# Optimization experiments

Hardware: AMD Instinct MI355X
Metric: run time of the kernel (lower is better)

Reference implementation:

```python
import jax, jax.numpy as jnp
import numpy as np

B, S, D = 8, 4096, 256
L, H = 4, 8
HD = D // H  # head_dim = 32
EPS = 1e-5


def layer_norm(x, gamma, beta):
    mu = jnp.mean(x, axis=-1, keepdims=True)
    var = jnp.mean(jnp.square(x - mu), axis=-1, keepdims=True)
    return (x - mu) * jax.lax.rsqrt(var + EPS) * gamma + beta


def setup_inputs() -> dict:
    key = jax.random.key(0)
    ks = jax.random.split(key, 9)
    sc = 0.02
    x = jax.random.normal(ks[0], (B, S, D), dtype=jnp.float32)
    # per-head projection weights, torch Linear convention: (out=head_dim, in=D)
    Wq = jax.random.normal(ks[1], (L, H, HD, D), dtype=jnp.float32) * sc
    Wk = jax.random.normal(ks[2], (L, H, HD, D), dtype=jnp.float32) * sc
    Wv = jax.random.normal(ks[3], (L, H, HD, D), dtype=jnp.float32) * sc
    W1 = jax.random.normal(ks[4], (L, D, D), dtype=jnp.float32) * sc
    b1 = jax.random.normal(ks[5], (L, D), dtype=jnp.float32) * sc
    W2 = jax.random.normal(ks[6], (L, D, D), dtype=jnp.float32) * sc
    b2 = jax.random.normal(ks[7], (L, D), dtype=jnp.float32) * sc
    gamma = jnp.ones((D,), dtype=jnp.float32)
    beta = jnp.zeros((D,), dtype=jnp.float32)
    return {"processed_grid_repr": x, "Wq": Wq, "Wk": Wk, "Wv": Wv,
            "W1": W1, "b1": b1, "W2": W2, "b2": b2,
            "gamma": gamma, "beta": beta}


def reference(processed_grid_repr, Wq, Wk, Wv, W1, b1, W2, b2, gamma, beta):
    out = processed_grid_repr  # (B, S, D)
    scale = 1.0 / jnp.sqrt(jnp.float32(S))  # original scales by sqrt(seq_len)
    for l in range(L):
        h = layer_norm(out, gamma, beta)
        # all heads at once: (B, H, S, HD)
        Q = jnp.einsum('bsd,hed->bhse', h, Wq[l])
        K = jnp.einsum('bsd,hed->bhse', h, Wk[l])
        V = jnp.einsum('bsd,hed->bhse', h, Wv[l])
        # original does key.reshape(B, HD, S) (a RESHAPE, not a transpose)
        Kr = K.reshape(B, H, HD, S)
        # original einsum 'bqq,bqd->bqd' only uses the diagonal of QK^r,
        # so compute only the diagonal: diag[b,h,q] = sum_e Q[b,h,q,e]*Kr[b,h,e,q]
        diag = jnp.einsum('bhse,bhes->bhs', Q, Kr) * scale
        attn = diag[..., None] * V  # (B, H, S, HD)
        # concat heads along last dim (head order preserved)
        msa_out = attn.transpose(0, 2, 1, 3).reshape(B, S, D)
        attended = msa_out + out
        m = layer_norm(attended, gamma, beta)
        m = jax.nn.gelu(m @ W1[l].T + b1[l], approximate=False)
        m = jax.nn.gelu(m @ W2[l].T + b2[l], approximate=False)
        out = m + attended
    # final: layer norm of CLS-like token 0
    return layer_norm(out[:, 0, :], gamma, beta)  # (B, D)
```

## Files before the change

kernel.cpp:

```cpp
#include <hip/hip_runtime.h>
#include <hip/hip_bf16.h>
#include <hip/hip_fp16.h>

typedef _Float16 half_t;
typedef _Float16 half8 __attribute__((ext_vector_type(8)));
typedef _Float16 half4 __attribute__((ext_vector_type(4)));
typedef float f32x4 __attribute__((ext_vector_type(4)));

#define BB 8
#define SS 4096
#define DD 256
#define HH 8
#define LL 4
#define MTOT (BB*SS)

__device__ inline float gelu_f(float v) { return 0.5f * v * (1.0f + erff(v * 0.70710678118f)); }

__device__ __forceinline__ void gload16(const half_t* g, half_t* l) {
    __builtin_amdgcn_global_load_lds(
        (const __attribute__((address_space(1))) void*)g,
        (__attribute__((address_space(3))) void*)l, 16, 0, 0);
}

__global__ __launch_bounds__(256) void prep_weights(
    const float* __restrict__ Wq, const float* __restrict__ Wk, const float* __restrict__ Wv,
    const float* __restrict__ W1, const float* __restrict__ b1,
    const float* __restrict__ W2, const float* __restrict__ b2,
    const float* __restrict__ gamma, const float* __restrict__ beta,
    half_t* __restrict__ Wall, half_t* __restrict__ W1h, half_t* __restrict__ W2h,
    float* __restrict__ bqkv, float* __restrict__ b1f, float* __restrict__ b2f)
{
    int blk = blockIdx.x;
    int l = blk / 5, type = blk % 5;
    int o = threadIdx.x;
    const float* src = (type == 0 ? Wq : type == 1 ? Wk : type == 2 ? Wv : type == 3 ? W1 : W2)
                       + ((size_t)l * 256 + o) * 256;
    half_t* dsth = (type < 3) ? Wall + ((size_t)(l * 3 + type) * 256 + o) * 256
                 : (type == 3) ? W1h + ((size_t)l * 256 + o) * 256
                               : W2h + ((size_t)l * 256 + o) * 256;
    float acc = 0.f;
    for (int d4 = 0; d4 < 64; ++d4) {
        float4 w = *(const float4*)(src + d4 * 4);
        half4 hv;
        if (type == 4) {
            hv = half4{ (half_t)w.x, (half_t)w.y, (half_t)w.z, (half_t)w.w };
        } else {
            float4 g = *(const float4*)(gamma + d4 * 4);
            float4 bt = *(const float4*)(beta + d4 * 4);
            acc += w.x * bt.x + w.y * bt.y + w.z * bt.z + w.w * bt.w;
            hv = half4{ (half_t)(w.x * g.x), (half_t)(w.y * g.y), (half_t)(w.z * g.z), (half_t)(w.w * g.w) };
        }
        *(half4*)(dsth + d4 * 4) = hv;
    }
    if (type < 3) bqkv[(l * 3 + type) * 256 + o] = acc;
    else if (type == 3) b1f[l * 256 + o] = b1[l * 256 + o] + acc;
    else b2f[l * 256 + o] = b2[l * 256 + o];
}

__global__ __launch_bounds__(256) void cvt_x(const float* __restrict__ in, half_t* __restrict__ out) {
    int i = (blockIdx.x * 256 + threadIdx.x) * 4;
    float4 v = *(const float4*)(in + i);
    half4 h = { (half_t)v.x, (half_t)v.y, (half_t)v.z, (half_t)v.w };
    *(half4*)(out + i) = h;
}

__global__ __launch_bounds__(256) void ln_z(const half_t* __restrict__ in, half_t* __restrict__ z) {
    int wave = threadIdx.x >> 6, lane = threadIdx.x & 63;
    int row = blockIdx.x * 4 + wave;
    size_t base = (size_t)row * DD + lane * 4;
    half4 x4 = *(const half4*)(in + base);
    float a0 = x4[0], a1 = x4[1], a2 = x4[2], a3 = x4[3];
    float s1 = a0 + a1 + a2 + a3;
    float s2 = a0 * a0 + a1 * a1 + a2 * a2 + a3 * a3;
    #pragma unroll
    for (int m = 32; m; m >>= 1) {
        s1 += __shfl_xor(s1, m);
        s2 += __shfl_xor(s2, m);
    }
    float mu = s1 * (1.0f / DD);
    float var = s2 * (1.0f / DD) - mu * mu;
    float rs = rsqrtf(var + 1e-5f);
    half4 o = { (half_t)((a0 - mu) * rs), (half_t)((a1 - mu) * rs),
                (half_t)((a2 - mu) * rs), (half_t)((a3 - mu) * rs) };
    *(half4*)(z + base) = o;
}

__device__ inline void xcd_remap(int& bx, int& by, int& bz) {
    int lin = blockIdx.x + gridDim.x * (blockIdx.y + gridDim.y * blockIdx.z);
    int nyz = gridDim.y * gridDim.z;
    int xcd = lin & 7;
    int slot = lin >> 3;
    int yz = slot % nyz;
    int xi = slot / nyz;
    bx = xcd + 8 * xi;
    by = yz % gridDim.y;
    bz = yz / gridDim.y;
}

template<int EPI>
__global__ __launch_bounds__(256) void gemm64(const half_t* __restrict__ A,
                                              const half_t* __restrict__ Wbase,
                                              const float* __restrict__ biasBase,
                                              const half_t* __restrict__ resid,
                                              half_t* __restrict__ o0,
                                              half_t* __restrict__ o1,
                                              half_t* __restrict__ o2) {
    const int t = threadIdx.x, lane = t & 63, wavei = t >> 6;
    const int wm = wavei >> 1, wn = wavei & 1, r = lane & 15, g = lane >> 4;
    int bx, by, bz;
    xcd_remap(bx, by, bz);
    const int row0 = bx * 64, col0 = by * 64;
    const half_t* W = Wbase + (size_t)bz * 65536;
    const float* bias = biasBase + bz * 256;
    half_t* outp = (bz == 0) ? o0 : ((bz == 1) ? o1 : o2);

    __shared__ __align__(16) half_t ldsA[2][4096];
    __shared__ __align__(16) half_t ldsB[2][4096];

    const half_t* Ag = A + (size_t)row0 * DD;
    const half_t* Wg = W + (size_t)col0 * DD;

    int rowS[2], chS[2];
    #pragma unroll
    for (int i = 0; i < 2; ++i) {
        int G = i * 256 + t;
        rowS[i] = G >> 3;
        chS[i] = ((G & 7) ^ (rowS[i] & 7)) * 8;
    }

    #pragma unroll
    for (int i = 0; i < 2; ++i) {
        int G = i * 256 + t;
        gload16(Ag + (size_t)rowS[i] * DD + chS[i], &ldsA[0][G * 8]);
        gload16(Wg + (size_t)rowS[i] * DD + chS[i], &ldsB[0][G * 8]);
    }
    __syncthreads();

    f32x4 acc[2][2];
    #pragma unroll
    for (int i = 0; i < 2; ++i)
        #pragma unroll
        for (int j = 0; j < 2; ++j) acc[i][j] = (f32x4){0.f, 0.f, 0.f, 0.f};

    #pragma unroll
    for (int stp = 0; stp < 4; ++stp) {
        const int cur = stp & 1;
        if (stp < 3) {
            int kk = (stp + 1) * 64;
            #pragma unroll
            for (int i = 0; i < 2; ++i) {
                int G = i * 256 + t;
                gload16(Ag + (size_t)rowS[i] * DD + kk + chS[i], &ldsA[cur ^ 1][G * 8]);
                gload16(Wg + (size_t)rowS[i] * DD + kk + chS[i], &ldsB[cur ^ 1][G * 8]);
            }
        }
        #pragma unroll
        for (int ks = 0; ks < 2; ++ks) {
            half8 af[2], bf[2];
            #pragma unroll
            for (int mt = 0; mt < 2; ++mt) {
                int rw = wm * 32 + mt * 16 + r;
                int cc = (ks * 4 + g) ^ (rw & 7);
                af[mt] = *(const half8*)&ldsA[cur][rw * 64 + cc * 8];
            }
            #pragma unroll
            for (int nt = 0; nt < 2; ++nt) {
                int rw = wn * 32 + nt * 16 + r;
                int cc = (ks * 4 + g) ^ (rw & 7);
                bf[nt] = *(const half8*)&ldsB[cur][rw * 64 + cc * 8];
            }
            #pragma unroll
            for (int mt = 0; mt < 2; ++mt)
                #pragma unroll
                for (int nt = 0; nt < 2; ++nt)
                    acc[mt][nt] = __builtin_amdgcn_mfma_f32_16x16x32_f16(af[mt], bf[nt], acc[mt][nt], 0, 0, 0);
        }
        __syncthreads();
    }

    half_t* ldsT = &ldsA[0][0];
    #pragma unroll
    for (int mt = 0; mt < 2; ++mt) {
        #pragma unroll
        for (int nt = 0; nt < 2; ++nt) {
            int colL = wn * 32 + nt * 16 + r;
            float bv = bias[col0 + colL];
            #pragma unroll
            for (int j = 0; j < 4; ++j) {
                int rowL = wm * 32 + mt * 16 + g * 4 + j;
                float v = acc[mt][nt][j] + bv;
                if (EPI != 0) v = gelu_f(v);
                ldsT[rowL * 64 + (((colL >> 3) ^ (rowL & 7)) << 3) + (colL & 7)] = (half_t)v;
            }
        }
    }
    __syncthreads();
    #pragma unroll
    for (int i = 0; i < 2; ++i) {
        int rowL = i * 32 + (t >> 3);
        int cc2 = t & 7;
        half8 v = *(const half8*)&ldsT[rowL * 64 + ((cc2 ^ (rowL & 7)) << 3)];
        size_t off = (size_t)(row0 + rowL) * DD + col0 + cc2 * 8;
        if (EPI == 2) {
            half8 rsd = *(const half8*)&resid[off];
            #pragma unroll
            for (int q = 0; q < 8; ++q) v[q] = (half_t)((float)v[q] + (float)rsd[q]);
        }
        *(half8*)&outp[off] = v;
    }
}

__global__ __launch_bounds__(256) void diag_tiled(const half_t* __restrict__ Q,
                                                  const half_t* __restrict__ K,
                                                  float* __restrict__ dg) {
    int blk = blockIdx.x;
    int sblk = blk & 15, h = (blk >> 4) & 7, b = blk >> 7;
    int t = threadIdx.x;
    __shared__ __align__(16) half_t kt[256 * 32];
    int r0b = sblk * 8;
    {
        int e = t >> 3, del = t & 7;
        const half_t* kp = K + ((size_t)b * SS + e * 128 + r0b + del) * DD + h * 32;
        int4* dst = (int4*)&kt[t * 32];
        const int4* sp = (const int4*)kp;
        dst[0] = sp[0]; dst[1] = sp[1]; dst[2] = sp[2]; dst[3] = sp[3];
    }
    __syncthreads();
    int s = sblk * 256 + t;
    const half8* q8 = (const half8*)(Q + ((size_t)b * SS + s) * DD + h * 32);
    int cs = t & 31, ds = t >> 5;
    float sum = 0.f;
    #pragma unroll
    for (int v = 0; v < 4; ++v) {
        half8 qq = q8[v];
        #pragma unroll
        for (int j = 0; j < 8; ++j) {
            int e = v * 8 + j;
            sum += (float)qq[j] * (float)kt[(e * 8 + ds) * 32 + cs];
        }
    }
    dg[((size_t)b << 15) | ((size_t)h << 12) | s] = sum * 0.015625f;
}

__global__ __launch_bounds__(256) void attn_ln16(const half_t* __restrict__ resid,
                                                 const half_t* __restrict__ V,
                                                 const float* __restrict__ dg,
                                                 half_t* __restrict__ att,
                                                 half_t* __restrict__ z2) {
    int wave = threadIdx.x >> 6, lane = threadIdx.x & 63;
    int row = blockIdx.x * 4 + wave;
    int b = row >> 12, s = row & (SS - 1);
    int h = lane >> 3;
    float dgv = dg[((size_t)b << 15) | ((size_t)h << 12) | s];
    size_t base = (size_t)row * DD + lane * 4;
    half4 rs4 = *(const half4*)(resid + base);
    half4 v4 = *(const half4*)(V + base);
    float a0 = (float)rs4[0] + dgv * (float)v4[0];
    float a1 = (float)rs4[1] + dgv * (float)v4[1];
    float a2 = (float)rs4[2] + dgv * (float)v4[2];
    float a3 = (float)rs4[3] + dgv * (float)v4[3];
    half4 at = { (half_t)a0, (half_t)a1, (half_t)a2, (half_t)a3 };
    *(half4*)(att + base) = at;
    float s1 = a0 + a1 + a2 + a3;
    float s2 = a0 * a0 + a1 * a1 + a2 * a2 + a3 * a3;
    #pragma unroll
    for (int m = 32; m; m >>= 1) {
        s1 += __shfl_xor(s1, m);
        s2 += __shfl_xor(s2, m);
    }
    float mu = s1 * (1.0f / DD);
    float var = s2 * (1.0f / DD) - mu * mu;
    float rsq = rsqrtf(var + 1e-5f);
    half4 o = { (half_t)((a0 - mu) * rsq), (half_t)((a1 - mu) * rsq),
                (half_t)((a2 - mu) * rsq), (half_t)((a3 - mu) * rsq) };
    *(half4*)(z2 + base) = o;
}

__global__ __launch_bounds__(256) void final_ln_kernel(const half_t* __restrict__ cur,
                                                       float* __restrict__ out,
                                                       const float* __restrict__ gamma,
                                                       const float* __restrict__ beta) {
    int b = blockIdx.x;
    int d = threadIdx.x;
    float x = (float)cur[(size_t)b * SS * DD + d];
    float s1 = x, s2 = x * x;
    #pragma unroll
    for (int m = 32; m; m >>= 1) {
        s1 += __shfl_xor(s1, m);
        s2 += __shfl_xor(s2, m);
    }
    __shared__ float ls1[4], ls2[4];
    int wave = threadIdx.x >> 6, lane = threadIdx.x & 63;
    if (lane == 0) { ls1[wave] = s1; ls2[wave] = s2; }
    __syncthreads();
    float t1 = ls1[0] + ls1[1] + ls1[2] + ls1[3];
    float t2 = ls2[0] + ls2[1] + ls2[2] + ls2[3];
    float mu = t1 * (1.0f / DD);
    float var = t2 * (1.0f / DD) - mu * mu;
    float rs = rsqrtf(var + 1e-5f);
    out[(size_t)b * DD + d] = (x - mu) * rs * gamma[d] + beta[d];
}

extern "C" void kernel_launch(void* const* d_in, const int* in_sizes, int n_in,
                              void* d_out, int out_size, void* d_ws, size_t ws_size,
                              hipStream_t stream) {
    const float* x     = (const float*)d_in[0];
    const float* Wq    = (const float*)d_in[1];
    const float* Wk    = (const float*)d_in[2];
    const float* Wv    = (const float*)d_in[3];
    const float* W1    = (const float*)d_in[4];
    const float* b1    = (const float*)d_in[5];
    const float* W2    = (const float*)d_in[6];
    const float* b2    = (const float*)d_in[7];
    const float* gamma = (const float*)d_in[8];
    const float* beta  = (const float*)d_in[9];

    char* p = (char*)d_ws;
    half_t* x16  = (half_t*)p; p += (size_t)MTOT * DD * 2;
    half_t* cur  = (half_t*)p; p += (size_t)MTOT * DD * 2;
    half_t* att  = (half_t*)p; p += (size_t)MTOT * DD * 2;
    half_t* z1   = (half_t*)p; p += (size_t)MTOT * DD * 2;
    half_t* z2   = (half_t*)p; p += (size_t)MTOT * DD * 2;
    half_t* Qb   = (half_t*)p; p += (size_t)MTOT * DD * 2;
    half_t* Kb   = (half_t*)p; p += (size_t)MTOT * DD * 2;
    half_t* Vb   = (half_t*)p; p += (size_t)MTOT * DD * 2;
    half_t* m1   = (half_t*)p; p += (size_t)MTOT * DD * 2;
    float*  dgp  = (float*)p;  p += (size_t)BB * HH * SS * 4;
    half_t* Wall = (half_t*)p; p += (size_t)LL * 3 * 65536 * 2;
    half_t* W1h  = (half_t*)p; p += (size_t)LL * 65536 * 2;
    half_t* W2h  = (half_t*)p; p += (size_t)LL * 65536 * 2;
    float*  bqkv = (float*)p;  p += (size_t)LL * 3 * 256 * 4;
    float*  b1f  = (float*)p;  p += (size_t)LL * 256 * 4;
    float*  b2f  = (float*)p;  p += (size_t)LL * 256 * 4;

    prep_weights<<<LL * 5, 256, 0, stream>>>(Wq, Wk, Wv, W1, b1, W2, b2, gamma, beta,
                                             Wall, W1h, W2h, bqkv, b1f, b2f);
    cvt_x<<<8192, 256, 0, stream>>>(x, x16);

    const half_t* curin = x16;
    for (int l = 0; l < LL; ++l) {
        ln_z<<<MTOT / 4, 256, 0, stream>>>(curin, z1);
        gemm64<0><<<dim3(512, 4, 3), 256, 0, stream>>>(
            z1, Wall + (size_t)l * 3 * 65536, bqkv + l * 3 * 256, nullptr, Qb, Kb, Vb);
        diag_tiled<<<1024, 256, 0, stream>>>(Qb, Kb, dgp);
        attn_ln16<<<MTOT / 4, 256, 0, stream>>>(curin, Vb, dgp, att, z2);
        gemm64<1><<<dim3(512, 4, 1), 256, 0, stream>>>(
            z2, W1h + (size_t)l * 65536, b1f + l * 256, nullptr, m1, m1, m1);
        gemm64<2><<<dim3(512, 4, 1), 256, 0, stream>>>(
            m1, W2h + (size_t)l * 65536, b2f + l * 256, att, cur, cur, cur);
        curin = cur;
    }
    final_ln_kernel<<<BB, 256, 0, stream>>>(cur, (float*)d_out, gamma, beta);
}
```

Before: 381.2 us.

## Enlarge GEMM tiles from 64x64 to 128x128 per workgroup

Replaces the 64x64 output-tile GEMM with a 128x128 tile, giving each wave a 64x64 sub-tile with 4x4 MFMA accumulators, and halves the grid in both dimensions. The goal is more operand reuse per LDS load and less redundant global traffic for A and W. The epilogue gains a new LDS swizzle and store mapping. In exchange it uses more registers and LDS (64KB), which lowers occupancy, and launches fewer workgroups (512 for the FFN GEMMs) on a GPU with many CUs.

After: 367.6 us. 3.6% less time.

```diff
diff --git a/kernel.cpp b/kernel.cpp
--- a/kernel.cpp
+++ b/kernel.cpp
@@ -98,49 +98,48 @@
 }
 
 template<int EPI>
-__global__ __launch_bounds__(256) void gemm64(const half_t* __restrict__ A,
-                                              const half_t* __restrict__ Wbase,
-                                              const float* __restrict__ biasBase,
-                                              const half_t* __restrict__ resid,
-                                              half_t* __restrict__ o0,
-                                              half_t* __restrict__ o1,
-                                              half_t* __restrict__ o2) {
+__global__ __launch_bounds__(256) void gemm128(const half_t* __restrict__ A,
+                                               const half_t* __restrict__ Wbase,
+                                               const float* __restrict__ biasBase,
+                                               const half_t* __restrict__ resid,
+                                               half_t* __restrict__ o0,
+                                               half_t* __restrict__ o1,
+                                               half_t* __restrict__ o2) {
     const int t = threadIdx.x, lane = t & 63, wavei = t >> 6;
     const int wm = wavei >> 1, wn = wavei & 1, r = lane & 15, g = lane >> 4;
     int bx, by, bz;
     xcd_remap(bx, by, bz);
-    const int row0 = bx * 64, col0 = by * 64;
+    const int row0 = bx * 128, col0 = by * 128;
     const half_t* W = Wbase + (size_t)bz * 65536;
     const float* bias = biasBase + bz * 256;
     half_t* outp = (bz == 0) ? o0 : ((bz == 1) ? o1 : o2);
 
-    __shared__ __align__(16) half_t ldsA[2][4096];
-    __shared__ __align__(16) half_t ldsB[2][4096];
+    __shared__ __align__(16) half_t lds[2][16384];
 
     const half_t* Ag = A + (size_t)row0 * DD;
     const half_t* Wg = W + (size_t)col0 * DD;
 
-    int rowS[2], chS[2];
-    #pragma unroll
-    for (int i = 0; i < 2; ++i) {
+    int rowS[4], chS[4];
+    #pragma unroll
+    for (int i = 0; i < 4; ++i) {
         int G = i * 256 + t;
         rowS[i] = G >> 3;
         chS[i] = ((G & 7) ^ (rowS[i] & 7)) * 8;
     }
 
     #pragma unroll
-    for (int i = 0; i < 2; ++i) {
+    for (int i = 0; i < 4; ++i) {
         int G = i * 256 + t;
-        gload16(Ag + (size_t)rowS[i] * DD + chS[i], &ldsA[0][G * 8]);
-        gload16(Wg + (size_t)rowS[i] * DD + chS[i], &ldsB[0][G * 8]);
+        gload16(Ag + (size_t)rowS[i] * DD + chS[i], &lds[0][G * 8]);
+        gload16(Wg + (size_t)rowS[i] * DD + chS[i], &lds[0][8192 + G * 8]);
     }
     __syncthreads();
 
-    f32x4 acc[2][2];
-    #pragma unroll
-    for (int i = 0; i < 2; ++i)
+    f32x4 acc[4][4];
+    #pragma unroll
+    for (int i = 0; i < 4; ++i)
         #pragma unroll
-        for (int j = 0; j < 2; ++j) acc[i][j] = (f32x4){0.f, 0.f, 0.f, 0.f};
+        for (int j = 0; j < 4; ++j) acc[i][j] = (f32x4){0.f, 0.f, 0.f, 0.f};
 
     #pragma unroll
     for (int stp = 0; stp < 4; ++stp) {
@@ -148,59 +147,60 @@
         if (stp < 3) {
             int kk = (stp + 1) * 64;
             #pragma unroll
-            for (int i = 0; i < 2; ++i) {
+            for (int i = 0; i < 4; ++i) {
                 int G = i * 256 + t;
-                gload16(Ag + (size_t)rowS[i] * DD + kk + chS[i], &ldsA[cur ^ 1][G * 8]);
-                gload16(Wg + (size_t)rowS[i] * DD + kk + chS[i], &ldsB[cur ^ 1][G * 8]);
+                gload16(Ag + (size_t)rowS[i] * DD + kk + chS[i], &lds[cur ^ 1][G * 8]);
+                gload16(Wg + (size_t)rowS[i] * DD + kk + chS[i], &lds[cur ^ 1][8192 + G * 8]);
             }
         }
         #pragma unroll
         for (int ks = 0; ks < 2; ++ks) {
-            half8 af[2], bf[2];
-            #pragma unroll
-            for (int mt = 0; mt < 2; ++mt) {
-                int rw = wm * 32 + mt * 16 + r;
+            half8 af[4], bf[4];
+            #pragma unroll
+            for (int mt = 0; mt < 4; ++mt) {
+                int rw = wm * 64 + mt * 16 + r;
                 int cc = (ks * 4 + g) ^ (rw & 7);
-                af[mt] = *(const half8*)&ldsA[cur][rw * 64 + cc * 8];
+                af[mt] = *(const half8*)&lds[cur][rw * 64 + cc * 8];
             }
             #pragma unroll
-            for (int nt = 0; nt < 2; ++nt) {
-                int rw = wn * 32 + nt * 16 + r;
+            for (int nt = 0; nt < 4; ++nt) {
+                int rw = wn * 64 + nt * 16 + r;
                 int cc = (ks * 4 + g) ^ (rw & 7);
-                bf[nt] = *(const half8*)&ldsB[cur][rw * 64 + cc * 8];
+                bf[nt] = *(const half8*)&lds[cur][8192 + rw * 64 + cc * 8];
             }
             #pragma unroll
-            for (int mt = 0; mt < 2; ++mt)
+            for (int mt = 0; mt < 4; ++mt)
                 #pragma unroll
-                for (int nt = 0; nt < 2; ++nt)
+                for (int nt = 0; nt < 4; ++nt)
                     acc[mt][nt] = __builtin_amdgcn_mfma_f32_16x16x32_f16(af[mt], bf[nt], acc[mt][nt], 0, 0, 0);
         }
         __syncthreads();
     }
 
-    half_t* ldsT = &ldsA[0][0];
-    #pragma unroll
-    for (int mt = 0; mt < 2; ++mt) {
+    half_t* ldsT = &lds[0][0];
+    #pragma unroll
+    for (int mt = 0; mt < 4; ++mt) {
         #pragma unroll
-        for (int nt = 0; nt < 2; ++nt) {
-            int colL = wn * 32 + nt * 16 + r;
+        for (int nt = 0; nt < 4; ++nt) {
+            int colL = wn * 64 + nt * 16 + r;
             float bv = bias[col0 + colL];
             #pragma unroll
             for (int j = 0; j < 4; ++j) {
-                int rowL = wm * 32 + mt * 16 + g * 4 + j;
+                int rowL = wm * 64 + mt * 16 + g * 4 + j;
                 float v = acc[mt][nt][j] + bv;
                 if (EPI != 0) v = gelu_f(v);
-                ldsT[rowL * 64 + (((colL >> 3) ^ (rowL & 7)) << 3) + (colL & 7)] = (half_t)v;
+                ldsT[rowL * 128 + (colL ^ ((rowL & 12) << 2))] = (half_t)v;
             }
         }
     }
     __syncthreads();
-    #pragma unroll
-    for (int i = 0; i < 2; ++i) {
-        int rowL = i * 32 + (t >> 3);
-        int cc2 = t & 7;
-        half8 v = *(const half8*)&ldsT[rowL * 64 + ((cc2 ^ (rowL & 7)) << 3)];
-        size_t off = (size_t)(row0 + rowL) * DD + col0 + cc2 * 8;
+    const int l15 = lane & 15, lg = lane >> 4;
+    #pragma unroll
+    for (int i = 0; i < 8; ++i) {
+        int rowL = wavei * 32 + lg * 8 + i;
+        int colL = l15 * 8;
+        half8 v = *(const half8*)&ldsT[rowL * 128 + (colL ^ ((rowL & 12) << 2))];
+        size_t off = (size_t)(row0 + rowL) * DD + col0 + colL;
         if (EPI == 2) {
             half8 rsd = *(const half8*)&resid[off];
             #pragma unroll
@@ -340,13 +340,13 @@
     const half_t* curin = x16;
     for (int l = 0; l < LL; ++l) {
         ln_z<<<MTOT / 4, 256, 0, stream>>>(curin, z1);
-        gemm64<0><<<dim3(512, 4, 3), 256, 0, stream>>>(
+        gemm128<0><<<dim3(256, 2, 3), 256, 0, stream>>>(
             z1, Wall + (size_t)l * 3 * 65536, bqkv + l * 3 * 256, nullptr, Qb, Kb, Vb);
         diag_tiled<<<1024, 256, 0, stream>>>(Qb, Kb, dgp);
         attn_ln16<<<MTOT / 4, 256, 0, stream>>>(curin, Vb, dgp, att, z2);
-        gemm64<1><<<dim3(512, 4, 1), 256, 0, stream>>>(
+        gemm128<1><<<dim3(256, 2, 1), 256, 0, stream>>>(
             z2, W1h + (size_t)l * 65536, b1f + l * 256, nullptr, m1, m1, m1);
-        gemm64<2><<<dim3(512, 4, 1), 256, 0, stream>>>(
+        gemm128<2><<<dim3(256, 2, 1), 256, 0, stream>>>(
             m1, W2h + (size_t)l * 65536, b2f + l * 256, att, cur, cur, cur);
         curin = cur;
     }
```
